# Kernel tuning notes

Hardware: AMD Instinct MI355X
Metric: run time of the kernel (lower is better)

## Reference

```python
import jax, jax.numpy as jnp
import numpy as np

B, C, H, E, K, QT = 256, 1024, 64, 64, 2, 20000

def _mlp(x, W1, b1, W2, b2):
    # GKT MLP (eval mode: dropout off; batch-norm omitted, see notes)
    return jax.nn.relu(jax.nn.relu(x @ W1 + b1) @ W2 + b2)

def setup_inputs() -> dict:
    key = jax.random.key(0)
    ks = jax.random.split(key, 30)
    s = 0.05  # weight scale to keep pre-clamp activations in a sane range
    xt = jax.random.uniform(ks[0], (B,), dtype=jnp.float32)
    qt = jax.random.randint(ks[1], (B,), 0, QT)
    ht = jax.random.normal(ks[2], (B, C, H), dtype=jnp.float32)
    # binary question->concept incidence, ~4 KCs per question, col 0 forced on
    oh = (jax.random.uniform(ks[3], (QT, C)) < 4.0 / C).astype(jnp.float32)
    oh = oh.at[:, 0].set(1.0)
    qt_kc_one_hot = jnp.concatenate([oh, jnp.zeros((1, C), jnp.float32)], axis=0)  # zero padding row
    kc_embeddings = jax.random.normal(ks[4], (C, E), dtype=jnp.float32) * 0.1
    graphs = jax.random.uniform(ks[5], (K, C, C), dtype=jnp.float32)  # graph_model output
    neigh_weight = jnp.float32(0.8)
    MI = H + E
    Ws1 = jax.random.normal(ks[6], (MI, H), jnp.float32) * s; bs1 = jnp.zeros((H,), jnp.float32)
    Ws2 = jax.random.normal(ks[7], (H, H), jnp.float32) * s;  bs2 = jnp.zeros((H,), jnp.float32)
    Wn1 = jax.random.normal(ks[8], (K, 2 * MI, H), jnp.float32) * s; bn1 = jnp.zeros((K, H), jnp.float32)
    Wn2 = jax.random.normal(ks[9], (K, H, H), jnp.float32) * s;      bn2 = jnp.zeros((K, H), jnp.float32)
    ea_w = jax.random.uniform(ks[10], (C,), dtype=jnp.float32)
    We = jax.random.normal(ks[11], (H, H), jnp.float32) * s; be = jnp.zeros((H,), jnp.float32)
    Wa = jax.random.normal(ks[12], (H, H), jnp.float32) * s; ba = jnp.zeros((H,), jnp.float32)
    W_ih = jax.random.normal(ks[13], (H, 3 * H), jnp.float32) * s; b_ih = jnp.zeros((3 * H,), jnp.float32)
    W_hh = jax.random.normal(ks[14], (H, 3 * H), jnp.float32) * s; b_hh = jnp.zeros((3 * H,), jnp.float32)
    Wp = jax.random.normal(ks[15], (H, 1), jnp.float32) * s; bp = jnp.zeros((1,), jnp.float32)
    return dict(xt=xt, qt=qt, ht=ht, qt_kc_one_hot=qt_kc_one_hot, kc_embeddings=kc_embeddings,
                graphs=graphs, neigh_weight=neigh_weight, Ws1=Ws1, bs1=bs1, Ws2=Ws2, bs2=bs2,
                Wn1=Wn1, bn1=bn1, Wn2=Wn2, bn2=bn2, ea_w=ea_w, We=We, be=be, Wa=Wa, ba=ba,
                W_ih=W_ih, b_ih=b_ih, W_hh=W_hh, b_hh=b_hh, Wp=Wp, bp=bp)

def reference(xt, qt, ht, qt_kc_one_hot, kc_embeddings, graphs, neigh_weight,
              Ws1, bs1, Ws2, bs2, Wn1, bn1, Wn2, bn2, ea_w, We, be, Wa, ba,
              W_ih, b_ih, W_hh, b_hh, Wp, bp):
    # ---- _aggregate: the fusion loops never write back, so tmp_ht = cat(ht, kc_emb)
    mask = qt_kc_one_hot[qt]                                   # [B, C] gather of binary incidence
    kc = jnp.broadcast_to(kc_embeddings[None], (mask.shape[0], C, E))
    tmp_ht = jnp.concatenate([ht, kc], axis=-1)                # [B, C, H+E]
    # ---- _agg_neighbors
    self_ht = tmp_ht * mask[..., None]
    self_feat = jnp.clip(_mlp(self_ht, Ws1, bs1, Ws2, bs2), -10.0, 10.0)
    neigh_ht = jnp.clip(jnp.concatenate([self_ht, tmp_ht], axis=-1), -5.0, 5.0)  # [B,C,2(H+E)]
    # bug-faithful adj: mean of graphs[k] rows over sample 0's active concepts
    a0 = mask[0]                                               # [C]
    denom = jnp.maximum(a0.sum(), 1.0)
    adj = jnp.clip(jnp.einsum('c,kcd->kd', a0, graphs) / denom, -5.0, 5.0)       # [K, C]
    nb = jax.vmap(lambda W1, b1, W2, b2: _mlp(neigh_ht, W1, b1, W2, b2))(Wn1, bn1, Wn2, bn2)
    nb = jnp.clip(nb, -5.0, 5.0)                               # [K, B, C, H]
    w = jnp.clip(neigh_weight, 0.1, 0.9)
    nf = jnp.clip(adj[0][None, :, None] * nb[0], -5.0, 5.0)
    for k in range(1, K):
        nf = jnp.clip(w * nf + (1.0 - w) * adj[k][None, :, None] * nb[k], -5.0, 5.0)
    m_next = jnp.clip(jnp.where(mask[..., None] > 0.5, self_feat, nf), -50.0, 50.0)
    # ---- erase-add gate
    g = ea_w[None, :, None]
    res = m_next - g * jax.nn.sigmoid(m_next @ We + be) * m_next + g * jnp.tanh(m_next @ Wa + ba)
    # ---- GRUCell over flattened (B*C) rows
    gi = res @ W_ih + b_ih
    gh = ht @ W_hh + b_hh
    ir, iz, in_ = jnp.split(gi, 3, axis=-1)
    hr, hz, hn = jnp.split(gh, 3, axis=-1)
    r = jax.nn.sigmoid(ir + hr)
    z = jax.nn.sigmoid(iz + hz)
    n = jnp.tanh(in_ + r * hn)
    h_next = (1.0 - z) * n + z * ht                            # [B, C, H]
    y = jax.nn.sigmoid(h_next @ Wp + bp)[..., 0]               # [B, C]
    return y
```

## Files before the change

kernel.cpp:

```cpp
#include <hip/hip_runtime.h>

#define DEVINL __device__ __forceinline__

typedef __bf16 bf16x8 __attribute__((ext_vector_type(8)));
typedef float  f32x4  __attribute__((ext_vector_type(4)));

static constexpr size_t kAdjOff  = 0;
static constexpr size_t kBiasOff = 8192;
static constexpr size_t kFragOff = 8192 + 786432;

static constexpr int FB_Wn1h0 = 0,  FB_Wn1h1 = 8,  FB_Wn2_0 = 16, FB_Wn2_1 = 24;
static constexpr int FB_Ws1h  = 32, FB_Ws2   = 40, FB_We    = 48, FB_Wa    = 56;
static constexpr int FB_Wih   = 64, FB_Whh   = 88;

DEVINL unsigned short bf16r(float f) {
  unsigned u = __builtin_bit_cast(unsigned, f);
  unsigned r = ((u >> 16) & 1u) + 0x7FFFu;
  return (unsigned short)((u + r) >> 16);
}
DEVINL float sigmoidf_(float x) { return __builtin_amdgcn_rcpf(1.f + __expf(-x)); }
DEVINL float tanhf_(float x)    { return 1.f - 2.f * __builtin_amdgcn_rcpf(1.f + __expf(2.f * x)); }

DEVINL void lds_fence() {
  __builtin_amdgcn_sched_barrier(0);
  __builtin_amdgcn_s_waitcnt(0xC07F);
  __builtin_amdgcn_sched_barrier(0);
}

DEVINL f32x4 mfma16(bf16x8 a, bf16x8 b, f32x4 c) {
  return __builtin_amdgcn_mfma_f32_16x16x32_bf16(a, b, c, 0, 0, 0);
}

DEVINL unsigned clip2_(unsigned x) {
  float lo = __builtin_bit_cast(float, x << 16);
  float hi = __builtin_bit_cast(float, x & 0xFFFF0000u);
  lo = fminf(fmaxf(lo, -5.f), 5.f);
  hi = fminf(fmaxf(hi, -5.f), 5.f);
  return (__builtin_bit_cast(unsigned, lo) >> 16) | (__builtin_bit_cast(unsigned, hi) & 0xFFFF0000u);
}
DEVINL bf16x8 clip5(bf16x8 a) {
  uint4 u = __builtin_bit_cast(uint4, a);
  u.x = clip2_(u.x); u.y = clip2_(u.y); u.z = clip2_(u.z); u.w = clip2_(u.w);
  return __builtin_bit_cast(bf16x8, u);
}

__global__ void prep_adj_kernel(const int* __restrict__ qt, const float* __restrict__ onehot,
                                const float* __restrict__ graphs, float* __restrict__ adjw) {
  __shared__ float a0v[1024];
  __shared__ int   aidx[1024];
  __shared__ int   s_nnz;
  __shared__ float s_den;
  const int tid = threadIdx.x;
  const int k = blockIdx.x >> 2, chunk = blockIdx.x & 3;
  if (tid == 0) { s_nnz = 0; s_den = 0.f; }
  __syncthreads();
  const int q0 = qt[0];
  float lsum = 0.f;
#pragma unroll
  for (int i = 0; i < 4; i++) {
    int c = tid * 4 + i;
    float v = onehot[(size_t)q0 * 1024 + c];
    lsum += v;
    if (v != 0.f) { int p = atomicAdd(&s_nnz, 1); aidx[p] = c; a0v[p] = v; }
  }
#pragma unroll
  for (int off = 32; off >= 1; off >>= 1) lsum += __shfl_xor(lsum, off, 64);
  if ((tid & 63) == 0) atomicAdd(&s_den, lsum);
  __syncthreads();
  const float denom = fmaxf(s_den, 1.f);
  const int nnz = s_nnz;
  const int d = chunk * 256 + tid;
  const float* G = graphs + (size_t)k * 1048576 + d;
  float sum = 0.f;
  for (int j = 0; j < nnz; j++) sum += a0v[j] * G[(size_t)aidx[j] * 1024];
  adjw[k * 1024 + d] = fminf(fmaxf(sum / denom, -5.f), 5.f);
}

__global__ void prep_bias_kernel(const float* __restrict__ kc, const float* __restrict__ Wn1,
                                 const float* __restrict__ bn1, const float* __restrict__ Ws1,
                                 const float* __restrict__ bs1, float* __restrict__ biasTab) {
  int gid = blockIdx.x * 256 + threadIdx.x;
  int j = gid & 63;
  int c = (gid >> 6) & 1023;
  int tab = gid >> 16;
  const float* kcr = kc + (size_t)c * 64;
  float s;
  if (tab < 2) {
    s = bn1[tab * 64 + j];
    const float* W = Wn1 + ((size_t)tab * 256 + 192) * 64 + j;
#pragma unroll 4
    for (int e = 0; e < 64; e++) s += fminf(fmaxf(kcr[e], -5.f), 5.f) * W[(size_t)e * 64];
  } else {
    s = bs1[j];
    const float* W = Ws1 + (size_t)64 * 64 + j;
#pragma unroll 4
    for (int e = 0; e < 64; e++) s += kcr[e] * W[(size_t)e * 64];
  }
  int c16 = c >> 4, rr = c & 3, qq = (c & 15) >> 2, nt = j >> 4;
  int lane = qq * 16 + (j & 15);
  biasTab[(size_t)((((c16 * 3 + tab) * 4 + nt) * 64 + lane)) * 4 + rr] = s;
}

__global__ void prep_wfrag_kernel(const float* __restrict__ Wn1, const float* __restrict__ Wn2,
                                  const float* __restrict__ Ws1, const float* __restrict__ Ws2,
                                  const float* __restrict__ We,  const float* __restrict__ Wa,
                                  const float* __restrict__ Wih, const float* __restrict__ Whh,
                                  uint4* __restrict__ wfrag) {
  const int bid = blockIdx.x, lane = threadIdx.x;
  int mat, ks, nt;
  if (bid < 64) { mat = bid >> 3; ks = (bid >> 2) & 1; nt = bid & 3; }
  else { int f2 = bid - 64; mat = 8 + f2 / 24; int f = f2 % 24; ks = f / 12; nt = f % 12; }
  const float* base = Wn1; int stride = 64;
  switch (mat) {
    case 0: base = Wn1 + (size_t)128 * 64; break;
    case 1: base = Wn1 + (size_t)(256 + 128) * 64; break;
    case 2: base = Wn2; break;
    case 3: base = Wn2 + (size_t)64 * 64; break;
    case 4: base = Ws1; break;
    case 5: base = Ws2; break;
    case 6: base = We; break;
    case 7: base = Wa; break;
    case 8: base = Wih; stride = 192; break;
    case 9: base = Whh; stride = 192; break;
  }
  const int qq = lane >> 4, col = nt * 16 + (lane & 15);
  union { unsigned short u[8]; uint4 v; } tmp;
#pragma unroll
  for (int jj = 0; jj < 8; jj++) {
    int k = ks * 32 + qq * 8 + jj;
    tmp.u[jj] = bf16r(base[(size_t)k * stride + col]);
  }
  wfrag[(size_t)bid * 64 + lane] = tmp.v;
}

__global__ __launch_bounds__(256, 3) void gkt_main_kernel(
    const int* __restrict__ qt, const float* __restrict__ onehot, const float* __restrict__ ht,
    const float* __restrict__ nw, const float* __restrict__ bn2, const float* __restrict__ be,
    const float* __restrict__ ba, const float* __restrict__ bih, const float* __restrict__ bhh,
    const float* __restrict__ Wp, const float* __restrict__ bp, const float* __restrict__ eaw,
    const float* __restrict__ bs2, const float* __restrict__ adjw, const float* __restrict__ biasTab,
    const bf16x8* __restrict__ wfrag, float* __restrict__ out) {
  __shared__ __align__(16) unsigned short hbuf[4][32][72];
  __shared__ __align__(16) float tokp[4][128];
  __shared__ __align__(16) uint4 gfrag[32 * 64];

  const int tid = threadIdx.x;
  const int wv = tid >> 6, lane = tid & 63;
  const int q = lane >> 4, cl = lane & 15;
  const int t0 = (blockIdx.x * 4 + wv) * 32;
  const int b = t0 >> 10, c0 = t0 & 1023, c16 = c0 >> 4;

  unsigned short* hb = &hbuf[wv][0][0];
  float* tp = &tokp[wv][0];

  {
    const uint4* wf4 = (const uint4*)wfrag;
#pragma unroll
    for (int i = 0; i < 8; i++) {
      int f = wv * 8 + i;
      gfrag[f * 64 + lane] = wf4[(64 + f) * 64 + lane];
    }
  }

  if (lane < 32) {
    const int c = c0 + lane;
    tp[lane]      = onehot[(size_t)qt[b] * 1024 + c];
    tp[32 + lane] = adjw[c];
    tp[64 + lane] = adjw[1024 + c];
    tp[96 + lane] = eaw[c];
  }
  {
    const float4* ht4 = (const float4*)ht;
#pragma unroll
    for (int i = 0; i < 8; i++) {
      float4 v = ht4[(size_t)t0 * 16 + i * 64 + lane];
      int e = i * 64 + lane;
      int tok = e >> 4, coll = (e & 15) * 4;
      ushort4 h;
      h.x = bf16r(v.x); h.y = bf16r(v.y); h.z = bf16r(v.z); h.w = bf16r(v.w);
      *(ushort4*)&hbuf[wv][tok][coll] = h;
    }
  }
  __syncthreads();

  const float wmix = fminf(fmaxf(nw[0], 0.1f), 0.9f);
  float wp4[4];
#pragma unroll
  for (int nt = 0; nt < 4; nt++) wp4[nt] = Wp[nt * 16 + cl];
  const float bpv = bp[0];

  auto ldA = [&](int mt, int ks) -> bf16x8 {
    return *(const bf16x8*)(hb + (cl + 16 * mt) * 72 + ks * 32 + q * 8);
  };
  auto ldB = [&](int frag) -> bf16x8 { return wfrag[frag * 64 + lane]; };
  auto ldG = [&](int fr) -> bf16x8 {
    return (fr < 32) ? *(const bf16x8*)&gfrag[fr * 64 + lane]
                     : wfrag[(64 + fr) * 64 + lane];
  };
  auto ldTP4 = [&](int base, int mt) -> f32x4 {
    return *(const f32x4*)(tp + base + 16 * mt + q * 4);
  };
  const f32x4* bt4 = (const f32x4*)biasTab;

  bf16x8 xr[2][2];
#pragma unroll
  for (int mt = 0; mt < 2; mt++)
#pragma unroll
    for (int ks = 0; ks < 2; ks++) xr[mt][ks] = ldA(mt, ks);
  lds_fence();

  f32x4 nf[2][4];
  {
    bf16x8 xc[2][2];
#pragma unroll
    for (int mt = 0; mt < 2; mt++)
#pragma unroll
      for (int ks = 0; ks < 2; ks++) xc[mt][ks] = clip5(xr[mt][ks]);

#pragma unroll
    for (int k2 = 0; k2 < 2; k2++) {
      f32x4 acc[2][4];
#pragma unroll
      for (int mt = 0; mt < 2; mt++)
#pragma unroll
        for (int nt = 0; nt < 4; nt++)
          acc[mt][nt] = bt4[(((c16 + mt) * 3 + k2) * 4 + nt) * 64 + lane];
#pragma unroll
      for (int ks = 0; ks < 2; ks++)
#pragma unroll
        for (int nt = 0; nt < 4; nt++) {
          bf16x8 bb = ldB((k2 ? FB_Wn1h1 : FB_Wn1h0) + ks * 4 + nt);
          acc[0][nt] = mfma16(xc[0][ks], bb, acc[0][nt]);
          acc[1][nt] = mfma16(xc[1][ks], bb, acc[1][nt]);
        }
#pragma unroll
      for (int mt = 0; mt < 2; mt++)
#pragma unroll
        for (int nt = 0; nt < 4; nt++)
#pragma unroll
          for (int r = 0; r < 4; r++)
            hb[(16 * mt + q * 4 + r) * 72 + nt * 16 + cl] = bf16r(fmaxf(acc[mt][nt][r], 0.f));
      lds_fence();
      f32x4 acc2[2][4];
#pragma unroll
      for (int nt = 0; nt < 4; nt++) {
        float bz = bn2[k2 * 64 + nt * 16 + cl];
        f32x4 iv = {bz, bz, bz, bz};
        acc2[0][nt] = iv; acc2[1][nt] = iv;
      }
#pragma unroll
      for (int ks = 0; ks < 2; ks++) {
        bf16x8 a0 = ldA(0, ks), a1 = ldA(1, ks);
#pragma unroll
        for (int nt = 0; nt < 4; nt++) {
          bf16x8 bb = ldB((k2 ? FB_Wn2_1 : FB_Wn2_0) + ks * 4 + nt);
          acc2[0][nt] = mfma16(a0, bb, acc2[0][nt]);
          acc2[1][nt] = mfma16(a1, bb, acc2[1][nt]);
        }
      }
      lds_fence();
#pragma unroll
      for (int mt = 0; mt < 2; mt++) {
        f32x4 adjv = ldTP4((1 + k2) * 32, mt);
#pragma unroll
        for (int nt = 0; nt < 4; nt++)
#pragma unroll
          for (int r = 0; r < 4; r++) {
            float nb = fminf(fmaxf(acc2[mt][nt][r], 0.f), 5.f);
            float v = adjv[r] * nb;
            if (k2 == 0) nf[mt][nt][r] = wmix * fminf(fmaxf(v, -5.f), 5.f);
            else         nf[mt][nt][r] = fminf(fmaxf(nf[mt][nt][r] + (1.f - wmix) * v, -5.f), 5.f);
          }
      }
    }
  }

  bool anySelf = __any((lane < 32) && (tp[lane] > 0.5f));
  if (anySelf) {
    f32x4 acc[2][4];
#pragma unroll
    for (int mt = 0; mt < 2; mt++)
#pragma unroll
      for (int nt = 0; nt < 4; nt++)
        acc[mt][nt] = bt4[(((c16 + mt) * 3 + 2) * 4 + nt) * 64 + lane];
#pragma unroll
    for (int ks = 0; ks < 2; ks++)
#pragma unroll
      for (int nt = 0; nt < 4; nt++) {
        bf16x8 bb = ldB(FB_Ws1h + ks * 4 + nt);
        acc[0][nt] = mfma16(xr[0][ks], bb, acc[0][nt]);
        acc[1][nt] = mfma16(xr[1][ks], bb, acc[1][nt]);
      }
#pragma unroll
    for (int mt = 0; mt < 2; mt++)
#pragma unroll
      for (int nt = 0; nt < 4; nt++)
#pragma unroll
        for (int r = 0; r < 4; r++)
          hb[(16 * mt + q * 4 + r) * 72 + nt * 16 + cl] = bf16r(fmaxf(acc[mt][nt][r], 0.f));
    lds_fence();
    f32x4 acc2[2][4];
#pragma unroll
    for (int nt = 0; nt < 4; nt++) {
      float bz = bs2[nt * 16 + cl];
      f32x4 iv = {bz, bz, bz, bz};
      acc2[0][nt] = iv; acc2[1][nt] = iv;
    }
#pragma unroll
    for (int ks = 0; ks < 2; ks++) {
      bf16x8 a0 = ldA(0, ks), a1 = ldA(1, ks);
#pragma unroll
      for (int nt = 0; nt < 4; nt++) {
        bf16x8 bb = ldB(FB_Ws2 + ks * 4 + nt);
        acc2[0][nt] = mfma16(a0, bb, acc2[0][nt]);
        acc2[1][nt] = mfma16(a1, bb, acc2[1][nt]);
      }
    }
    lds_fence();
#pragma unroll
    for (int mt = 0; mt < 2; mt++) {
      f32x4 mk = ldTP4(0, mt);
#pragma unroll
      for (int nt = 0; nt < 4; nt++)
#pragma unroll
        for (int r = 0; r < 4; r++) {
          float sf = fminf(fmaxf(acc2[mt][nt][r], 0.f), 10.f);
          nf[mt][nt][r] = (mk[r] > 0.5f) ? sf : nf[mt][nt][r];
        }
    }
  }

#pragma unroll
  for (int mt = 0; mt < 2; mt++)
#pragma unroll
    for (int nt = 0; nt < 4; nt++)
#pragma unroll
      for (int r = 0; r < 4; r++)
        hb[(16 * mt + q * 4 + r) * 72 + nt * 16 + cl] = bf16r(nf[mt][nt][r]);
  lds_fence();
  bf16x8 mf[2][2];
#pragma unroll
  for (int mt = 0; mt < 2; mt++)
#pragma unroll
    for (int ks = 0; ks < 2; ks++) mf[mt][ks] = ldA(mt, ks);
  lds_fence();
  {
    f32x4 accE[2][4];
#pragma unroll
    for (int nt = 0; nt < 4; nt++) {
      float bz = be[nt * 16 + cl];
      f32x4 iv = {bz, bz, bz, bz};
      accE[0][nt] = iv; accE[1][nt] = iv;
    }
#pragma unroll
    for (int ks = 0; ks < 2; ks++)
#pragma unroll
      for (int nt = 0; nt < 4; nt++) {
        bf16x8 bb = ldB(FB_We + ks * 4 + nt);
        accE[0][nt] = mfma16(mf[0][ks], bb, accE[0][nt]);
        accE[1][nt] = mfma16(mf[1][ks], bb, accE[1][nt]);
      }
#pragma unroll
    for (int mt = 0; mt < 2; mt++) {
      f32x4 gv = ldTP4(96, mt);
#pragma unroll
      for (int nt = 0; nt < 4; nt++)
#pragma unroll
        for (int r = 0; r < 4; r++) {
          float m = nf[mt][nt][r];
          nf[mt][nt][r] = m - gv[r] * sigmoidf_(accE[mt][nt][r]) * m;
        }
    }
    f32x4 accA[2][4];
#pragma unroll
    for (int nt = 0; nt < 4; nt++) {
      float bz = ba[nt * 16 + cl];
      f32x4 iv = {bz, bz, bz, bz};
      accA[0][nt] = iv; accA[1][nt] = iv;
    }
#pragma unroll
    for (int ks = 0; ks < 2; ks++)
#pragma unroll
      for (int nt = 0; nt < 4; nt++) {
        bf16x8 bb = ldB(FB_Wa + ks * 4 + nt);
        accA[0][nt] = mfma16(mf[0][ks], bb, accA[0][nt]);
        accA[1][nt] = mfma16(mf[1][ks], bb, accA[1][nt]);
      }
#pragma unroll
    for (int mt = 0; mt < 2; mt++) {
      f32x4 gv = ldTP4(96, mt);
#pragma unroll
      for (int nt = 0; nt < 4; nt++)
#pragma unroll
        for (int r = 0; r < 4; r++)
          nf[mt][nt][r] += gv[r] * tanhf_(accA[mt][nt][r]);
    }
  }

#pragma unroll
  for (int mt = 0; mt < 2; mt++)
#pragma unroll
    for (int nt = 0; nt < 4; nt++)
#pragma unroll
      for (int r = 0; r < 4; r++)
        hb[(16 * mt + q * 4 + r) * 72 + nt * 16 + cl] = bf16r(nf[mt][nt][r]);
  lds_fence();
  bf16x8 rf[2][2];
#pragma unroll
  for (int mt = 0; mt < 2; mt++)
#pragma unroll
    for (int ks = 0; ks < 2; ks++) rf[mt][ks] = ldA(mt, ks);

#pragma unroll
  for (int mt = 0; mt < 2; mt++) {
    f32x4 gR[4], gZ[4], gN[4], gH[4];
#pragma unroll
    for (int nt = 0; nt < 4; nt++) {
      int col = nt * 16 + cl;
      float brz = bih[col] + bhh[col];
      float bzz = bih[64 + col] + bhh[64 + col];
      float bnn = bih[128 + col];
      float bhn = bhh[128 + col];
      gR[nt] = {brz, brz, brz, brz};
      gZ[nt] = {bzz, bzz, bzz, bzz};
      gN[nt] = {bnn, bnn, bnn, bnn};
      gH[nt] = {bhn, bhn, bhn, bhn};
    }
#pragma unroll
    for (int ks = 0; ks < 2; ks++)
#pragma unroll
      for (int nt = 0; nt < 4; nt++) {
        bf16x8 bi_r = ldG(ks * 12 + nt);
        bf16x8 bh_r = ldG(24 + ks * 12 + nt);
        bf16x8 bi_z = ldG(ks * 12 + 4 + nt);
        bf16x8 bh_z = ldG(24 + ks * 12 + 4 + nt);
        bf16x8 bi_n = ldG(ks * 12 + 8 + nt);
        bf16x8 bh_n = ldG(24 + ks * 12 + 8 + nt);
        gR[nt] = mfma16(rf[mt][ks], bi_r, gR[nt]);
        gR[nt] = mfma16(xr[mt][ks], bh_r, gR[nt]);
        gZ[nt] = mfma16(rf[mt][ks], bi_z, gZ[nt]);
        gZ[nt] = mfma16(xr[mt][ks], bh_z, gZ[nt]);
        gN[nt] = mfma16(rf[mt][ks], bi_n, gN[nt]);
        gH[nt] = mfma16(xr[mt][ks], bh_n, gH[nt]);
      }

#pragma unroll
    for (int r = 0; r < 4; r++) {
      int tok = 16 * mt + q * 4 + r;
      float part = 0.f;
#pragma unroll
      for (int nt = 0; nt < 4; nt++) {
        float rr = sigmoidf_(gR[nt][r]);
        float zz = sigmoidf_(gZ[nt][r]);
        float nval = tanhf_(gN[nt][r] + rr * gH[nt][r]);
        float htv = ht[(size_t)(t0 + tok) * 64 + nt * 16 + cl];
        float hnx = (1.f - zz) * nval + zz * htv;
        part += hnx * wp4[nt];
      }
      part += __shfl_xor(part, 1, 64);
      part += __shfl_xor(part, 2, 64);
      part += __shfl_xor(part, 4, 64);
      part += __shfl_xor(part, 8, 64);
      if (cl == 0) out[t0 + tok] = sigmoidf_(part + bpv);
    }
  }
}

extern "C" void kernel_launch(void* const* d_in, const int* in_sizes, int n_in,
                              void* d_out, int out_size, void* d_ws, size_t ws_size,
                              hipStream_t stream) {
  const int*   qt     = (const int*)d_in[1];
  const float* ht     = (const float*)d_in[2];
  const float* onehot = (const float*)d_in[3];
  const float* kc     = (const float*)d_in[4];
  const float* graphs = (const float*)d_in[5];
  const float* nw     = (const float*)d_in[6];
  const float* Ws1    = (const float*)d_in[7];
  const float* bs1    = (const float*)d_in[8];
  const float* Ws2    = (const float*)d_in[9];
  const float* bs2    = (const float*)d_in[10];
  const float* Wn1    = (const float*)d_in[11];
  const float* bn1    = (const float*)d_in[12];
  const float* Wn2    = (const float*)d_in[13];
  const float* bn2    = (const float*)d_in[14];
  const float* eaw    = (const float*)d_in[15];
  const float* We     = (const float*)d_in[16];
  const float* be     = (const float*)d_in[17];
  const float* Wa     = (const float*)d_in[18];
  const float* ba     = (const float*)d_in[19];
  const float* Wih    = (const float*)d_in[20];
  const float* bih    = (const float*)d_in[21];
  const float* Whh    = (const float*)d_in[22];
  const float* bhh    = (const float*)d_in[23];
  const float* Wp     = (const float*)d_in[24];
  const float* bp     = (const float*)d_in[25];
  float* out = (float*)d_out;

  float* adjw    = (float*)((char*)d_ws + kAdjOff);
  float* biasTab = (float*)((char*)d_ws + kBiasOff);
  uint4* wfragU  = (uint4*)((char*)d_ws + kFragOff);

  prep_adj_kernel<<<8, 256, 0, stream>>>(qt, onehot, graphs, adjw);
  prep_bias_kernel<<<768, 256, 0, stream>>>(kc, Wn1, bn1, Ws1, bs1, biasTab);
  prep_wfrag_kernel<<<112, 64, 0, stream>>>(Wn1, Wn2, Ws1, Ws2, We, Wa, Wih, Whh, wfragU);
  gkt_main_kernel<<<2048, 256, 0, stream>>>(qt, onehot, ht, nw, bn2, be, ba, bih, bhh,
                                            Wp, bp, eaw, bs2, adjw, biasTab,
                                            (const bf16x8*)wfragU, out);
}
```

Before: 283.3 us.

## Halve per-wave token tile to 16 rows and stage more GRU fragments in LDS

Each wave now handles 16 tokens instead of 32, doubling the grid to 4096 blocks and dropping the second M-tile from every matmul stage, which cuts register and LDS use per wave. The freed LDS is used to stage 40 rather than 32 GRU weight fragments, so fewer are read from global memory. In exchange, each weight fragment loaded is reused across half as many rows, and per-block setup (fragment staging, token parameter loads) is repeated over twice as many blocks.

```diff
diff --git a/kernel.cpp b/kernel.cpp
--- a/kernel.cpp
+++ b/kernel.cpp
@@ -140,14 +140,14 @@
     const float* __restrict__ Wp, const float* __restrict__ bp, const float* __restrict__ eaw,
     const float* __restrict__ bs2, const float* __restrict__ adjw, const float* __restrict__ biasTab,
     const bf16x8* __restrict__ wfrag, float* __restrict__ out) {
-  __shared__ __align__(16) unsigned short hbuf[4][32][72];
-  __shared__ __align__(16) float tokp[4][128];
-  __shared__ __align__(16) uint4 gfrag[32 * 64];
+  __shared__ __align__(16) unsigned short hbuf[4][16][72];
+  __shared__ __align__(16) float tokp[4][64];
+  __shared__ __align__(16) uint4 gfrag[40 * 64];
 
   const int tid = threadIdx.x;
   const int wv = tid >> 6, lane = tid & 63;
   const int q = lane >> 4, cl = lane & 15;
-  const int t0 = (blockIdx.x * 4 + wv) * 32;
+  const int t0 = (blockIdx.x * 4 + wv) * 16;
   const int b = t0 >> 10, c0 = t0 & 1023, c16 = c0 >> 4;
 
   unsigned short* hb = &hbuf[wv][0][0];
@@ -156,23 +156,23 @@
   {
     const uint4* wf4 = (const uint4*)wfrag;
 #pragma unroll
-    for (int i = 0; i < 8; i++) {
-      int f = wv * 8 + i;
+    for (int i = 0; i < 10; i++) {
+      int f = wv * 10 + i;
       gfrag[f * 64 + lane] = wf4[(64 + f) * 64 + lane];
     }
   }
 
-  if (lane < 32) {
+  if (lane < 16) {
     const int c = c0 + lane;
     tp[lane]      = onehot[(size_t)qt[b] * 1024 + c];
-    tp[32 + lane] = adjw[c];
-    tp[64 + lane] = adjw[1024 + c];
-    tp[96 + lane] = eaw[c];
+    tp[16 + lane] = adjw[c];
+    tp[32 + lane] = adjw[1024 + c];
+    tp[48 + lane] = eaw[c];
   }
   {
     const float4* ht4 = (const float4*)ht;
 #pragma unroll
-    for (int i = 0; i < 8; i++) {
+    for (int i = 0; i < 4; i++) {
       float4 v = ht4[(size_t)t0 * 16 + i * 64 + lane];
       int e = i * 64 + lane;
       int tok = e >> 4, coll = (e & 15) * 4;
@@ -184,285 +184,247 @@
   __syncthreads();
 
   const float wmix = fminf(fmaxf(nw[0], 0.1f), 0.9f);
-  float wp4[4];
-#pragma unroll
-  for (int nt = 0; nt < 4; nt++) wp4[nt] = Wp[nt * 16 + cl];
-  const float bpv = bp[0];
-
-  auto ldA = [&](int mt, int ks) -> bf16x8 {
-    return *(const bf16x8*)(hb + (cl + 16 * mt) * 72 + ks * 32 + q * 8);
+
+  auto ldA = [&](int ks) -> bf16x8 {
+    return *(const bf16x8*)(hb + cl * 72 + ks * 32 + q * 8);
   };
   auto ldB = [&](int frag) -> bf16x8 { return wfrag[frag * 64 + lane]; };
   auto ldG = [&](int fr) -> bf16x8 {
-    return (fr < 32) ? *(const bf16x8*)&gfrag[fr * 64 + lane]
+    return (fr < 40) ? *(const bf16x8*)&gfrag[fr * 64 + lane]
                      : wfrag[(64 + fr) * 64 + lane];
   };
-  auto ldTP4 = [&](int base, int mt) -> f32x4 {
-    return *(const f32x4*)(tp + base + 16 * mt + q * 4);
+  auto ldTP4 = [&](int base) -> f32x4 {
+    return *(const f32x4*)(tp + base + q * 4);
   };
   const f32x4* bt4 = (const f32x4*)biasTab;
 
-  bf16x8 xr[2][2];
-#pragma unroll
-  for (int mt = 0; mt < 2; mt++)
-#pragma unroll
-    for (int ks = 0; ks < 2; ks++) xr[mt][ks] = ldA(mt, ks);
+  bf16x8 xr[2];
+#pragma unroll
+  for (int ks = 0; ks < 2; ks++) xr[ks] = ldA(ks);
   lds_fence();
 
-  f32x4 nf[2][4];
+  f32x4 nf[4];
   {
-    bf16x8 xc[2][2];
-#pragma unroll
-    for (int mt = 0; mt < 2; mt++)
-#pragma unroll
-      for (int ks = 0; ks < 2; ks++) xc[mt][ks] = clip5(xr[mt][ks]);
-
 #pragma unroll
     for (int k2 = 0; k2 < 2; k2++) {
-      f32x4 acc[2][4];
-#pragma unroll
-      for (int mt = 0; mt < 2; mt++)
-#pragma unroll
-        for (int nt = 0; nt < 4; nt++)
-          acc[mt][nt] = bt4[(((c16 + mt) * 3 + k2) * 4 + nt) * 64 + lane];
-#pragma unroll
-      for (int ks = 0; ks < 2; ks++)
+      f32x4 acc[4];
+#pragma unroll
+      for (int nt = 0; nt < 4; nt++)
+        acc[nt] = bt4[((c16 * 3 + k2) * 4 + nt) * 64 + lane];
+#pragma unroll
+      for (int ks = 0; ks < 2; ks++) {
+        bf16x8 xcv = clip5(xr[ks]);
 #pragma unroll
         for (int nt = 0; nt < 4; nt++) {
           bf16x8 bb = ldB((k2 ? FB_Wn1h1 : FB_Wn1h0) + ks * 4 + nt);
-          acc[0][nt] = mfma16(xc[0][ks], bb, acc[0][nt]);
-          acc[1][nt] = mfma16(xc[1][ks], bb, acc[1][nt]);
+          acc[nt] = mfma16(xcv, bb, acc[nt]);
         }
-#pragma unroll
-      for (int mt = 0; mt < 2; mt++)
-#pragma unroll
-        for (int nt = 0; nt < 4; nt++)
-#pragma unroll
-          for (int r = 0; r < 4; r++)
-            hb[(16 * mt + q * 4 + r) * 72 + nt * 16 + cl] = bf16r(fmaxf(acc[mt][nt][r], 0.f));
+      }
+#pragma unroll
+      for (int nt = 0; nt < 4; nt++)
+#pragma unroll
+        for (int r = 0; r < 4; r++)
+          hb[(q * 4 + r) * 72 + nt * 16 + cl] = bf16r(fmaxf(acc[nt][r], 0.f));
       lds_fence();
-      f32x4 acc2[2][4];
+      f32x4 acc2[4];
 #pragma unroll
       for (int nt = 0; nt < 4; nt++) {
         float bz = bn2[k2 * 64 + nt * 16 + cl];
-        f32x4 iv = {bz, bz, bz, bz};
-        acc2[0][nt] = iv; acc2[1][nt] = iv;
+        acc2[nt] = {bz, bz, bz, bz};
       }
 #pragma unroll
       for (int ks = 0; ks < 2; ks++) {
-        bf16x8 a0 = ldA(0, ks), a1 = ldA(1, ks);
+        bf16x8 a0 = ldA(ks);
 #pragma unroll
         for (int nt = 0; nt < 4; nt++) {
           bf16x8 bb = ldB((k2 ? FB_Wn2_1 : FB_Wn2_0) + ks * 4 + nt);
-          acc2[0][nt] = mfma16(a0, bb, acc2[0][nt]);
-          acc2[1][nt] = mfma16(a1, bb, acc2[1][nt]);
+          acc2[nt] = mfma16(a0, bb, acc2[nt]);
         }
       }
       lds_fence();
-#pragma unroll
-      for (int mt = 0; mt < 2; mt++) {
-        f32x4 adjv = ldTP4((1 + k2) * 32, mt);
+      {
+        f32x4 adjv = ldTP4((1 + k2) * 16);
 #pragma unroll
         for (int nt = 0; nt < 4; nt++)
 #pragma unroll
           for (int r = 0; r < 4; r++) {
-            float nb = fminf(fmaxf(acc2[mt][nt][r], 0.f), 5.f);
+            float nb = fminf(fmaxf(acc2[nt][r], 0.f), 5.f);
             float v = adjv[r] * nb;
-            if (k2 == 0) nf[mt][nt][r] = wmix * fminf(fmaxf(v, -5.f), 5.f);
-            else         nf[mt][nt][r] = fminf(fmaxf(nf[mt][nt][r] + (1.f - wmix) * v, -5.f), 5.f);
+            if (k2 == 0) nf[nt][r] = wmix * fminf(fmaxf(v, -5.f), 5.f);
+            else         nf[nt][r] = fminf(fmaxf(nf[nt][r] + (1.f - wmix) * v, -5.f), 5.f);
           }
       }
     }
   }
 
-  bool anySelf = __any((lane < 32) && (tp[lane] > 0.5f));
+  bool anySelf = __any((lane < 16) && (tp[lane] > 0.5f));
   if (anySelf) {
-    f32x4 acc[2][4];
-#pragma unroll
-    for (int mt = 0; mt < 2; mt++)
-#pragma unroll
-      for (int nt = 0; nt < 4; nt++)
-        acc[mt][nt] = bt4[(((c16 + mt) * 3 + 2) * 4 + nt) * 64 + lane];
+    f32x4 acc[4];
+#pragma unroll
+    for (int nt = 0; nt < 4; nt++)
+      acc[nt] = bt4[((c16 * 3 + 2) * 4 + nt) * 64 + lane];
 #pragma unroll
     for (int ks = 0; ks < 2; ks++)
 #pragma unroll
       for (int nt = 0; nt < 4; nt++) {
         bf16x8 bb = ldB(FB_Ws1h + ks * 4 + nt);
-        acc[0][nt] = mfma16(xr[0][ks], bb, acc[0][nt]);
-        acc[1][nt] = mfma16(xr[1][ks], bb, acc[1][nt]);
-      }
-#pragma unroll
-    for (int mt = 0; mt < 2; mt++)
-#pragma unroll
-      for (int nt = 0; nt < 4; nt++)
-#pragma unroll
-        for (int r = 0; r < 4; r++)
-          hb[(16 * mt + q * 4 + r) * 72 + nt * 16 + cl] = bf16r(fmaxf(acc[mt][nt][r], 0.f));
+        acc[nt] = mfma16(xr[ks], bb, acc[nt]);
+      }
+#pragma unroll
+    for (int nt = 0; nt < 4; nt++)
+#pragma unroll
+      for (int r = 0; r < 4; r++)
+        hb[(q * 4 + r) * 72 + nt * 16 + cl] = bf16r(fmaxf(acc[nt][r], 0.f));
     lds_fence();
-    f32x4 acc2[2][4];
+    f32x4 acc2[4];
 #pragma unroll
     for (int nt = 0; nt < 4; nt++) {
       float bz = bs2[nt * 16 + cl];
-      f32x4 iv = {bz, bz, bz, bz};
-      acc2[0][nt] = iv; acc2[1][nt] = iv;
+      acc2[nt] = {bz, bz, bz, bz};
     }
 #pragma unroll
     for (int ks = 0; ks < 2; ks++) {
-      bf16x8 a0 = ldA(0, ks), a1 = ldA(1, ks);
+      bf16x8 a0 = ldA(ks);
 #pragma unroll
       for (int nt = 0; nt < 4; nt++) {
         bf16x8 bb = ldB(FB_Ws2 + ks * 4 + nt);
-        acc2[0][nt] = mfma16(a0, bb, acc2[0][nt]);
-        acc2[1][nt] = mfma16(a1, bb, acc2[1][nt]);
+        acc2[nt] = mfma16(a0, bb, acc2[nt]);
       }
     }
     lds_fence();
-#pragma unroll
-    for (int mt = 0; mt < 2; mt++) {
-      f32x4 mk = ldTP4(0, mt);
+    {
+      f32x4 mk = ldTP4(0);
 #pragma unroll
       for (int nt = 0; nt < 4; nt++)
 #pragma unroll
         for (int r = 0; r < 4; r++) {
-          float sf = fminf(fmaxf(acc2[mt][nt][r], 0.f), 10.f);
-          nf[mt][nt][r] = (mk[r] > 0.5f) ? sf : nf[mt][nt][r];
+          float sf = fminf(fmaxf(acc2[nt][r], 0.f), 10.f);
+          nf[nt][r] = (mk[r] > 0.5f) ? sf : nf[nt][r];
         }
     }
   }
 
 #pragma unroll
-  for (int mt = 0; mt < 2; mt++)
-#pragma unroll
-    for (int nt = 0; nt < 4; nt++)
-#pragma unroll
-      for (int r = 0; r < 4; r++)
-        hb[(16 * mt + q * 4 + r) * 72 + nt * 16 + cl] = bf16r(nf[mt][nt][r]);
+  for (int nt = 0; nt < 4; nt++)
+#pragma unroll
+    for (int r = 0; r < 4; r++)
+      hb[(q * 4 + r) * 72 + nt * 16 + cl] = bf16r(nf[nt][r]);
   lds_fence();
-  bf16x8 mf[2][2];
-#pragma unroll
-  for (int mt = 0; mt < 2; mt++)
-#pragma unroll
-    for (int ks = 0; ks < 2; ks++) mf[mt][ks] = ldA(mt, ks);
+  bf16x8 mf[2];
+#pragma unroll
+  for (int ks = 0; ks < 2; ks++) mf[ks] = ldA(ks);
   lds_fence();
   {
-    f32x4 accE[2][4];
+    f32x4 accE[4];
 #pragma unroll
     for (int nt = 0; nt < 4; nt++) {
       float bz = be[nt * 16 + cl];
-      f32x4 iv = {bz, bz, bz, bz};
-      accE[0][nt] = iv; accE[1][nt] = iv;
+      accE[nt] = {bz, bz, bz, bz};
     }
 #pragma unroll
     for (int ks = 0; ks < 2; ks++)
 #pragma unroll
       for (int nt = 0; nt < 4; nt++) {
         bf16x8 bb = ldB(FB_We + ks * 4 + nt);
-        accE[0][nt] = mfma16(mf[0][ks], bb, accE[0][nt]);
-        accE[1][nt] = mfma16(mf[1][ks], bb, accE[1][nt]);
-      }
-#pragma unroll
-    for (int mt = 0; mt < 2; mt++) {
-      f32x4 gv = ldTP4(96, mt);
+        accE[nt] = mfma16(mf[ks], bb, accE[nt]);
+      }
+    {
+      f32x4 gv = ldTP4(48);
 #pragma unroll
       for (int nt = 0; nt < 4; nt++)
 #pragma unroll
         for (int r = 0; r < 4; r++) {
-          float m = nf[mt][nt][r];
-          nf[mt][nt][r] = m - gv[r] * sigmoidf_(accE[mt][nt][r]) * m;
+          float m = nf[nt][r];
+          nf[nt][r] = m - gv[r] * sigmoidf_(accE[nt][r]) * m;
         }
     }
-    f32x4 accA[2][4];
+    f32x4 accA[4];
 #pragma unroll
     for (int nt = 0; nt < 4; nt++) {
       float bz = ba[nt * 16 + cl];
-      f32x4 iv = {bz, bz, bz, bz};
-      accA[0][nt] = iv; accA[1][nt] = iv;
+      accA[nt] = {bz, bz, bz, bz};
     }
 #pragma unroll
     for (int ks = 0; ks < 2; ks++)
 #pragma unroll
       for (int nt = 0; nt < 4; nt++) {
         bf16x8 bb = ldB(FB_Wa + ks * 4 + nt);
-        accA[0][nt] = mfma16(mf[0][ks], bb, accA[0][nt]);
-        accA[1][nt] = mfma16(mf[1][ks], bb, accA[1][nt]);
-      }
-#pragma unroll
-    for (int mt = 0; mt < 2; mt++) {
-      f32x4 gv = ldTP4(96, mt);
+        accA[nt] = mfma16(mf[ks], bb, accA[nt]);
+      }
+    {
+      f32x4 gv = ldTP4(48);
 #pragma unroll
       for (int nt = 0; nt < 4; nt++)
 #pragma unroll
         for (int r = 0; r < 4; r++)
-          nf[mt][nt][r] += gv[r] * tanhf_(accA[mt][nt][r]);
-    }
-  }
-
-#pragma unroll
-  for (int mt = 0; mt < 2; mt++)
-#pragma unroll
-    for (int nt = 0; nt < 4; nt++)
-#pragma unroll
-      for (int r = 0; r < 4; r++)
-        hb[(16 * mt + q * 4 + r) * 72 + nt * 16 + cl] = bf16r(nf[mt][nt][r]);
+          nf[nt][r] += gv[r] * tanhf_(accA[nt][r]);
+    }
+  }
+
+#pragma unroll
+  for (int nt = 0; nt < 4; nt++)
+#pragma unroll
+    for (int r = 0; r < 4; r++)
+      hb[(q * 4 + r) * 72 + nt * 16 + cl] = bf16r(nf[nt][r]);
   lds_fence();
-  bf16x8 rf[2][2];
-#pragma unroll
-  for (int mt = 0; mt < 2; mt++)
-#pragma unroll
-    for (int ks = 0; ks < 2; ks++) rf[mt][ks] = ldA(mt, ks);
-
-#pragma unroll
-  for (int mt = 0; mt < 2; mt++) {
-    f32x4 gR[4], gZ[4], gN[4], gH[4];
+  bf16x8 rf[2];
+#pragma unroll
+  for (int ks = 0; ks < 2; ks++) rf[ks] = ldA(ks);
+
+  f32x4 gR[4], gZ[4], gN[4], gH[4];
+#pragma unroll
+  for (int nt = 0; nt < 4; nt++) {
+    int col = nt * 16 + cl;
+    float brz = bih[col] + bhh[col];
+    float bzz = bih[64 + col] + bhh[64 + col];
+    float bnn = bih[128 + col];
+    float bhn = bhh[128 + col];
+    gR[nt] = {brz, brz, brz, brz};
+    gZ[nt] = {bzz, bzz, bzz, bzz};
+    gN[nt] = {bnn, bnn, bnn, bnn};
+    gH[nt] = {bhn, bhn, bhn, bhn};
+  }
+#pragma unroll
+  for (int ks = 0; ks < 2; ks++)
 #pragma unroll
     for (int nt = 0; nt < 4; nt++) {
-      int col = nt * 16 + cl;
-      float brz = bih[col] + bhh[col];
-      float bzz = bih[64 + col] + bhh[64 + col];
-      float bnn = bih[128 + col];
-      float bhn = bhh[128 + col];
-      gR[nt] = {brz, brz, brz, brz};
-      gZ[nt] = {bzz, bzz, bzz, bzz};
-      gN[nt] = {bnn, bnn, bnn, bnn};
-      gH[nt] = {bhn, bhn, bhn, bhn};
-    }
-#pragma unroll
-    for (int ks = 0; ks < 2; ks++)
-#pragma unroll
-      for (int nt = 0; nt < 4; nt++) {
-        bf16x8 bi_r = ldG(ks * 12 + nt);
-        bf16x8 bh_r = ldG(24 + ks * 12 + nt);
-        bf16x8 bi_z = ldG(ks * 12 + 4 + nt);
-        bf16x8 bh_z = ldG(24 + ks * 12 + 4 + nt);
-        bf16x8 bi_n = ldG(ks * 12 + 8 + nt);
-        bf16x8 bh_n = ldG(24 + ks * 12 + 8 + nt);
-        gR[nt] = mfma16(rf[mt][ks], bi_r, gR[nt]);
-        gR[nt] = mfma16(xr[mt][ks], bh_r, gR[nt]);
-        gZ[nt] = mfma16(rf[mt][ks], bi_z, gZ[nt]);
-        gZ[nt] = mfma16(xr[mt][ks], bh_z, gZ[nt]);
-        gN[nt] = mfma16(rf[mt][ks], bi_n, gN[nt]);
-        gH[nt] = mfma16(xr[mt][ks], bh_n, gH[nt]);
-      }
-
-#pragma unroll
-    for (int r = 0; r < 4; r++) {
-      int tok = 16 * mt + q * 4 + r;
-      float part = 0.f;
-#pragma unroll
-      for (int nt = 0; nt < 4; nt++) {
-        float rr = sigmoidf_(gR[nt][r]);
-        float zz = sigmoidf_(gZ[nt][r]);
-        float nval = tanhf_(gN[nt][r] + rr * gH[nt][r]);
-        float htv = ht[(size_t)(t0 + tok) * 64 + nt * 16 + cl];
-        float hnx = (1.f - zz) * nval + zz * htv;
-        part += hnx * wp4[nt];
-      }
-      part += __shfl_xor(part, 1, 64);
-      part += __shfl_xor(part, 2, 64);
-      part += __shfl_xor(part, 4, 64);
-      part += __shfl_xor(part, 8, 64);
-      if (cl == 0) out[t0 + tok] = sigmoidf_(part + bpv);
-    }
+      bf16x8 bi_r = ldG(ks * 12 + nt);
+      bf16x8 bh_r = ldG(24 + ks * 12 + nt);
+      bf16x8 bi_z = ldG(ks * 12 + 4 + nt);
+      bf16x8 bh_z = ldG(24 + ks * 12 + 4 + nt);
+      bf16x8 bi_n = ldG(ks * 12 + 8 + nt);
+      bf16x8 bh_n = ldG(24 + ks * 12 + 8 + nt);
+      gR[nt] = mfma16(rf[ks], bi_r, gR[nt]);
+      gR[nt] = mfma16(xr[ks], bh_r, gR[nt]);
+      gZ[nt] = mfma16(rf[ks], bi_z, gZ[nt]);
+      gZ[nt] = mfma16(xr[ks], bh_z, gZ[nt]);
+      gN[nt] = mfma16(rf[ks], bi_n, gN[nt]);
+      gH[nt] = mfma16(xr[ks], bh_n, gH[nt]);
+    }
+
+  float wp4[4];
+#pragma unroll
+  for (int nt = 0; nt < 4; nt++) wp4[nt] = Wp[nt * 16 + cl];
+  const float bpv = bp[0];
+
+#pragma unroll
+  for (int r = 0; r < 4; r++) {
+    int tok = q * 4 + r;
+    float part = 0.f;
+#pragma unroll
+    for (int nt = 0; nt < 4; nt++) {
+      float rr = sigmoidf_(gR[nt][r]);
+      float zz = sigmoidf_(gZ[nt][r]);
+      float nval = tanhf_(gN[nt][r] + rr * gH[nt][r]);
+      float htv = ht[(size_t)(t0 + tok) * 64 + nt * 16 + cl];
+      float hnx = (1.f - zz) * nval + zz * htv;
+      part += hnx * wp4[nt];
+    }
+    part += __shfl_xor(part, 1, 64);
+    part += __shfl_xor(part, 2, 64);
+    part += __shfl_xor(part, 4, 64);
+    part += __shfl_xor(part, 8, 64);
+    if (cl == 0) out[t0 + tok] = sigmoidf_(part + bpv);
   }
 }
 
@@ -503,7 +465,7 @@
   prep_adj_kernel<<<8, 256, 0, stream>>>(qt, onehot, graphs, adjw);
   prep_bias_kernel<<<768, 256, 0, stream>>>(kc, Wn1, bn1, Ws1, bs1, biasTab);
   prep_wfrag_kernel<<<112, 64, 0, stream>>>(Wn1, Wn2, Ws1, Ws2, We, Wa, Wih, Whh, wfragU);
-  gkt_main_kernel<<<2048, 256, 0, stream>>>(qt, onehot, ht, nw, bn2, be, ba, bih, bhh,
+  gkt_main_kernel<<<4096, 256, 0, stream>>>(qt, onehot, ht, nw, bn2, be, ba, bih, bhh,
                                             Wp, bp, eaw, bs2, adjw, biasTab,
                                             (const bf16x8*)wfragU, out);
 }
```

Result: faster. 268.2 us (-5.3%).
